# Optimization experiments

Hardware: AMD Instinct MI355X
Metric: run time of the kernel (lower is better)

## Reference

```python
import jax, jax.numpy as jnp
from jax import lax
import numpy as np

N_MACRO, HIDDEN, N_LAYERS, N_REGIMES, N_ASSETS = 16, 256, 2, 3, 32
VIX_THRESHOLD, DEFENSIVE_ALLOC, EPSILON = 30.0, 0.4, 1e-8
N_EQ = 24  # equities = assets[:24], defensive = assets[24:]
N_DEF = N_ASSETS - N_EQ
LN_EPS = 1e-5


def setup_inputs() -> dict:
    key = jax.random.key(0)
    ks = jax.random.split(key, 16)
    B, S = 128, 1024
    inp = {
        'macro_features': jax.random.normal(ks[0], (B, S, N_MACRO), jnp.float32),
        'vix_values': jax.random.uniform(ks[1], (B,), jnp.float32) * 60.0,  # some above threshold
    }
    k = 1.0 / np.sqrt(HIDDEN)
    def u(kk, shape):
        return jax.random.uniform(kk, shape, jnp.float32, -k, k)
    # layer 0
    inp['lstm_Wih0'] = u(ks[2], (4 * HIDDEN, N_MACRO))
    inp['lstm_Whh0'] = u(ks[3], (4 * HIDDEN, HIDDEN))
    inp['lstm_bih0'] = u(ks[4], (4 * HIDDEN,))
    inp['lstm_bhh0'] = u(ks[5], (4 * HIDDEN,))
    # layer 1
    inp['lstm_Wih1'] = u(ks[6], (4 * HIDDEN, HIDDEN))
    inp['lstm_Whh1'] = u(ks[7], (4 * HIDDEN, HIDDEN))
    inp['lstm_bih1'] = u(ks[8], (4 * HIDDEN,))
    inp['lstm_bhh1'] = u(ks[9], (4 * HIDDEN,))
    inp['ln_gamma'] = jnp.ones((HIDDEN,), jnp.float32)
    inp['ln_beta'] = jnp.zeros((HIDDEN,), jnp.float32)
    inp['logits_W'] = u(ks[10], (N_REGIMES, HIDDEN))
    inp['logits_b'] = u(ks[11], (N_REGIMES,))
    inp['risk_budgets'] = jax.random.normal(ks[12], (N_REGIMES, N_ASSETS), jnp.float32) * 0.01
    return inp


def _lstm_layer(x, Wih, Whh, bih, bhh):
    # x: [B,S,I] -> h sequence [B,S,H]
    B = x.shape[0]
    H = Whh.shape[1]
    pre = jnp.einsum('bsi,gi->bsg', x, Wih) + bih + bhh  # [B,S,4H]
    def step(carry, p):
        h, c = carry
        g = p + h @ Whh.T
        i, f, gg, o = jnp.split(g, 4, axis=-1)
        c = jax.nn.sigmoid(f) * c + jax.nn.sigmoid(i) * jnp.tanh(gg)
        h = jax.nn.sigmoid(o) * jnp.tanh(c)
        return (h, c), h
    init = (jnp.zeros((B, H), x.dtype), jnp.zeros((B, H), x.dtype))
    _, hs = lax.scan(step, init, jnp.swapaxes(pre, 0, 1))
    return jnp.swapaxes(hs, 0, 1)


def _vix_override(beta, vix_mask):
    # vectorized version of the per-sample override loop
    eq, df = beta[:, :N_EQ], beta[:, N_EQ:]
    cur_def = df.sum(-1)
    shortfall = DEFENSIVE_ALLOC - cur_def
    eq_total = eq.sum(-1)
    ratio = jnp.minimum(shortfall / jnp.maximum(eq_total, EPSILON), 0.8)
    apply = vix_mask & (shortfall > 0) & (eq_total > EPSILON)
    new_eq = eq * (1.0 - ratio)[:, None]
    new_df = df + (shortfall / N_DEF)[:, None]
    b2 = jnp.concatenate([new_eq, new_df], axis=-1)
    b = jnp.where(apply[:, None], b2, beta)
    b_norm = b / (b.sum(-1, keepdims=True) + EPSILON)
    return jnp.where(vix_mask[:, None], b_norm, beta)


def reference(macro_features, vix_values,
              lstm_Wih0, lstm_Whh0, lstm_bih0, lstm_bhh0,
              lstm_Wih1, lstm_Whh1, lstm_bih1, lstm_bhh1,
              ln_gamma, ln_beta, logits_W, logits_b, risk_budgets):
    h1 = _lstm_layer(macro_features, lstm_Wih0, lstm_Whh0, lstm_bih0, lstm_bhh0)
    h2 = _lstm_layer(h1, lstm_Wih1, lstm_Whh1, lstm_bih1, lstm_bhh1)
    h_last = h2[:, -1, :]  # [B,H]
    mu = h_last.mean(-1, keepdims=True)
    var = ((h_last - mu) ** 2).mean(-1, keepdims=True)
    h_norm = (h_last - mu) / jnp.sqrt(var + LN_EPS) * ln_gamma + ln_beta
    regime_probs = jax.nn.softmax(h_norm @ logits_W.T + logits_b, axis=-1)  # [B,K]
    budgets = jax.nn.softmax(risk_budgets, axis=-1)  # [K,P]
    beta = jnp.einsum('bk,kp->bp', regime_probs, budgets)
    vix_mask = vix_values >= VIX_THRESHOLD
    beta = _vix_override(beta, vix_mask)
    return beta, regime_probs
```

## Files before the change

### kernel.cpp

```cpp
#include <hip/hip_runtime.h>

#define B_  128
#define S_  1024
#define H_  256
#define NM_ 16

typedef short bf16x8 __attribute__((ext_vector_type(8)));
typedef float f32x4  __attribute__((ext_vector_type(4)));

__device__ __forceinline__ short f2bf(float f) {
    unsigned u = __builtin_bit_cast(unsigned, f);
    unsigned r = (u + 0x7FFFu + ((u >> 16) & 1u)) >> 16;
    return (short)r;
}
__device__ __forceinline__ bf16x8 zero8() {
    bf16x8 v;
    #pragma unroll
    for (int j = 0; j < 8; ++j) v[j] = 0;
    return v;
}
__device__ __forceinline__ float sigf(float x)  { return 1.0f / (1.0f + __expf(-x)); }
__device__ __forceinline__ float tanh_(float x) { return 1.0f - 2.0f / (1.0f + __expf(2.0f * x)); }

__device__ __forceinline__ int cload_int(const int* p) {
    int r;
    asm volatile("global_load_dword %0, %1, off sc0 sc1\n\ts_waitcnt vmcnt(0)"
                 : "=v"(r) : "v"(p) : "memory");
    return r;
}
__device__ __forceinline__ void cstore_int(int* p, int v) {
    asm volatile("global_store_dword %0, %1, off sc0 sc1" :: "v"(p), "v"(v) : "memory");
}
__device__ __forceinline__ void cstore_short(short* p, int v) {
    asm volatile("global_store_short %0, %1, off sc0 sc1" :: "v"(p), "v"(v) : "memory");
}
__device__ __forceinline__ void vm_drain() {
    asm volatile("s_waitcnt vmcnt(0)" ::: "memory");
}
__device__ __forceinline__ void cload8x16(const short* p, bf16x8* d) {
    int4 a0, a1, a2, a3, a4, a5, a6, a7;
    asm volatile(
        "global_load_dwordx4 %0, %8, off sc0 sc1\n\t"
        "global_load_dwordx4 %1, %8, off offset:64 sc0 sc1\n\t"
        "global_load_dwordx4 %2, %8, off offset:128 sc0 sc1\n\t"
        "global_load_dwordx4 %3, %8, off offset:192 sc0 sc1\n\t"
        "global_load_dwordx4 %4, %8, off offset:256 sc0 sc1\n\t"
        "global_load_dwordx4 %5, %8, off offset:320 sc0 sc1\n\t"
        "global_load_dwordx4 %6, %8, off offset:384 sc0 sc1\n\t"
        "global_load_dwordx4 %7, %8, off offset:448 sc0 sc1\n\t"
        "s_waitcnt vmcnt(0)"
        : "=&v"(a0), "=&v"(a1), "=&v"(a2), "=&v"(a3),
          "=&v"(a4), "=&v"(a5), "=&v"(a6), "=&v"(a7)
        : "v"(p) : "memory");
    d[0] = __builtin_bit_cast(bf16x8, a0); d[1] = __builtin_bit_cast(bf16x8, a1);
    d[2] = __builtin_bit_cast(bf16x8, a2); d[3] = __builtin_bit_cast(bf16x8, a3);
    d[4] = __builtin_bit_cast(bf16x8, a4); d[5] = __builtin_bit_cast(bf16x8, a5);
    d[6] = __builtin_bit_cast(bf16x8, a6); d[7] = __builtin_bit_cast(bf16x8, a7);
}

__global__ __launch_bounds__(256, 1) void lstm_kernel(
    const float* __restrict__ x,
    const float* __restrict__ Wih0, const float* __restrict__ Whh0,
    const float* __restrict__ bih0, const float* __restrict__ bhh0,
    const float* __restrict__ Wih1, const float* __restrict__ Whh1,
    const float* __restrict__ bih1, const float* __restrict__ bhh1,
    short* __restrict__ h1, short* __restrict__ h2ring,
    float* __restrict__ hlast,
    int* __restrict__ flags0, int* __restrict__ flags1)
{
    const int g    = blockIdx.x & 7;
    const int role = blockIdx.x >> 3;
    const int lane = threadIdx.x & 63;
    const int wv   = threadIdx.x >> 6;
    const int n    = lane & 15;
    const int quad = lane >> 4;

    if (role < 4) {
        const int q = role;
        const int hu_base = q * 64 + wv * 16;
        bf16x8 wf[4][9];
        float  bias[4];
        #pragma unroll
        for (int G = 0; G < 4; ++G) {
            int col = G * 256 + hu_base + n;
            bias[G] = bih0[col] + bhh0[col];
            #pragma unroll
            for (int kt = 0; kt < 8; ++kt) {
                const float* p = Whh0 + (long)col * H_ + kt * 32 + quad * 8;
                bf16x8 v;
                #pragma unroll
                for (int j = 0; j < 8; ++j) v[j] = f2bf(p[j]);
                wf[G][kt] = v;
            }
            bf16x8 v = zero8();
            if (quad < 2) {
                const float* p = Wih0 + (long)col * NM_ + quad * 8;
                #pragma unroll
                for (int j = 0; j < 8; ++j) v[j] = f2bf(p[j]);
            }
            wf[G][8] = v;
        }
        const int  bRow = g * 16 + n;
        const long hA   = (long)bRow * S_ * H_ + quad * 8;
        f32x4 c = {0.f, 0.f, 0.f, 0.f};
        int* fl = flags0 + g * 4;
        for (int t = 0; t < S_; ++t) {
            bf16x8 xfrag = zero8();
            if (quad < 2) {
                const float* p = x + ((long)bRow * S_ + t) * NM_ + quad * 8;
                #pragma unroll
                for (int j = 0; j < 8; ++j) xfrag[j] = f2bf(p[j]);
            }
            if (threadIdx.x < 4) {
                while (cload_int(fl + threadIdx.x) < t) __builtin_amdgcn_s_sleep(1);
            }
            __syncthreads();

            bf16x8 af[9];
            if (t > 0) {
                cload8x16(h1 + hA + (long)(t - 1) * H_, af);
            } else {
                #pragma unroll
                for (int kt = 0; kt < 8; ++kt) af[kt] = zero8();
            }
            af[8] = xfrag;

            f32x4 acc[4];
            #pragma unroll
            for (int G = 0; G < 4; ++G) {
                acc[G][0] = bias[G]; acc[G][1] = bias[G];
                acc[G][2] = bias[G]; acc[G][3] = bias[G];
            }
            #pragma unroll
            for (int kt = 0; kt < 9; ++kt)
                #pragma unroll
                for (int G = 0; G < 4; ++G)
                    acc[G] = __builtin_amdgcn_mfma_f32_16x16x32_bf16(af[kt], wf[G][kt], acc[G], 0, 0, 0);
            #pragma unroll
            for (int r = 0; r < 4; ++r) {
                float iv = sigf(acc[0][r]);
                float fv = sigf(acc[1][r]);
                float gv = tanh_(acc[2][r]);
                float ov = sigf(acc[3][r]);
                c[r] = fv * c[r] + iv * gv;
                float hv = ov * tanh_(c[r]);
                int b = g * 16 + quad * 4 + r;
                cstore_short(h1 + ((long)b * S_ + t) * H_ + hu_base + n, (int)(unsigned short)f2bf(hv));
            }
            vm_drain();
            __syncthreads();
            if (threadIdx.x == 0) cstore_int(fl + q, t + 1);
        }
    } else {
        const int q = role - 4;
        const int hu_base = q * 64 + wv * 16;
        bf16x8 wf[4][16];
        float  bias[4];
        #pragma unroll
        for (int G = 0; G < 4; ++G) {
            int col = G * 256 + hu_base + n;
            bias[G] = bih1[col] + bhh1[col];
            #pragma unroll
            for (int kt = 0; kt < 8; ++kt) {
                const float* p = Whh1 + (long)col * H_ + kt * 32 + quad * 8;
                bf16x8 v;
                #pragma unroll
                for (int j = 0; j < 8; ++j) v[j] = f2bf(p[j]);
                wf[G][kt] = v;
            }
            #pragma unroll
            for (int kt = 0; kt < 8; ++kt) {
                const float* p = Wih1 + (long)col * H_ + kt * 32 + quad * 8;
                bf16x8 v;
                #pragma unroll
                for (int j = 0; j < 8; ++j) v[j] = f2bf(p[j]);
                wf[G][8 + kt] = v;
            }
        }
        const int  bRow = g * 16 + n;
        const long h1A  = (long)bRow * S_ * H_ + quad * 8;
        f32x4 c = {0.f, 0.f, 0.f, 0.f};
        int* fl0 = flags0 + g * 4;
        int* fl1 = flags1 + g * 4;
        for (int t = 0; t < S_; ++t) {
            if (threadIdx.x < 8) {
                const int* fp = (threadIdx.x < 4) ? (fl0 + threadIdx.x) : (fl1 + threadIdx.x - 4);
                const int  tgt = (threadIdx.x < 4) ? (t + 1) : t;
                while (cload_int(fp) < tgt) __builtin_amdgcn_s_sleep(1);
            }
            __syncthreads();

            bf16x8 af[16];
            if (t > 0) {
                cload8x16(h2ring + ((long)bRow * 2 + ((t - 1) & 1)) * H_ + quad * 8, af);
            } else {
                #pragma unroll
                for (int kt = 0; kt < 8; ++kt) af[kt] = zero8();
            }
            cload8x16(h1 + h1A + (long)t * H_, af + 8);

            f32x4 acc[4];
            #pragma unroll
            for (int G = 0; G < 4; ++G) {
                acc[G][0] = bias[G]; acc[G][1] = bias[G];
                acc[G][2] = bias[G]; acc[G][3] = bias[G];
            }
            #pragma unroll
            for (int kt = 0; kt < 16; ++kt)
                #pragma unroll
                for (int G = 0; G < 4; ++G)
                    acc[G] = __builtin_amdgcn_mfma_f32_16x16x32_bf16(af[kt], wf[G][kt], acc[G], 0, 0, 0);
            #pragma unroll
            for (int r = 0; r < 4; ++r) {
                float iv = sigf(acc[0][r]);
                float fv = sigf(acc[1][r]);
                float gv = tanh_(acc[2][r]);
                float ov = sigf(acc[3][r]);
                c[r] = fv * c[r] + iv * gv;
                float hv = ov * tanh_(c[r]);
                int b = g * 16 + quad * 4 + r;
                cstore_short(h2ring + ((long)b * 2 + (t & 1)) * H_ + hu_base + n,
                             (int)(unsigned short)f2bf(hv));
                if (t == S_ - 1) hlast[b * H_ + hu_base + n] = hv;
            }
            vm_drain();
            __syncthreads();
            if (threadIdx.x == 0) cstore_int(fl1 + q, t + 1);
        }
    }
}

__device__ __forceinline__ float blockSum(float v, float* sbuf) {
    #pragma unroll
    for (int off = 32; off > 0; off >>= 1) v += __shfl_down(v, off, 64);
    __syncthreads();
    if ((threadIdx.x & 63) == 0) sbuf[threadIdx.x >> 6] = v;
    __syncthreads();
    return sbuf[0] + sbuf[1] + sbuf[2] + sbuf[3];
}

__global__ __launch_bounds__(256) void tail_kernel(
    const float* __restrict__ hlast, const float* __restrict__ gamma,
    const float* __restrict__ lnbeta, const float* __restrict__ Wl,
    const float* __restrict__ bl, const float* __restrict__ rb,
    const float* __restrict__ vix, float* __restrict__ out)
{
    __shared__ float sbuf[4];
    __shared__ float pr[3], mxs[3], dens[3];
    __shared__ float bvec[32];
    const int b   = blockIdx.x;
    const int tid = threadIdx.x;

    float v  = hlast[b * H_ + tid];
    float mu = blockSum(v, sbuf) * (1.0f / 256.0f);
    float d  = v - mu;
    float var = blockSum(d * d, sbuf) * (1.0f / 256.0f);
    float hn  = d * rsqrtf(var + 1e-5f) * gamma[tid] + lnbeta[tid];

    float l[3];
    #pragma unroll
    for (int k = 0; k < 3; ++k)
        l[k] = blockSum(hn * Wl[k * H_ + tid], sbuf) + bl[k];

    if (tid == 0) {
        float m  = fmaxf(l[0], fmaxf(l[1], l[2]));
        float e0 = __expf(l[0] - m), e1 = __expf(l[1] - m), e2 = __expf(l[2] - m);
        float dn = e0 + e1 + e2;
        pr[0] = e0 / dn; pr[1] = e1 / dn; pr[2] = e2 / dn;
    }
    if (tid < 3) {
        float m = -1e30f;
        for (int p = 0; p < 32; ++p) m = fmaxf(m, rb[tid * 32 + p]);
        float dn = 0.f;
        for (int p = 0; p < 32; ++p) dn += __expf(rb[tid * 32 + p] - m);
        mxs[tid] = m; dens[tid] = dn;
    }
    __syncthreads();
    if (tid < 32) {
        float bp = 0.f;
        #pragma unroll
        for (int k = 0; k < 3; ++k)
            bp += pr[k] * __expf(rb[k * 32 + tid] - mxs[k]) / dens[k];
        bvec[tid] = bp;
    }
    __syncthreads();
    if (tid == 0) {
        bool  mask = vix[b] >= 30.0f;
        float eq_total = 0.f, cur_def = 0.f;
        for (int p = 0; p < 24; ++p) eq_total += bvec[p];
        for (int p = 24; p < 32; ++p) cur_def += bvec[p];
        float shortfall = 0.4f - cur_def;
        float ratio = fminf(shortfall / fmaxf(eq_total, 1e-8f), 0.8f);
        bool  apply = mask && (shortfall > 0.0f) && (eq_total > 1e-8f);
        float bb[32]; float ssum = 0.f;
        for (int p = 0; p < 32; ++p) {
            float b2 = (p < 24) ? bvec[p] * (1.0f - ratio) : bvec[p] + shortfall * (1.0f / 8.0f);
            float bv = apply ? b2 : bvec[p];
            bb[p] = bv; ssum += bv;
        }
        float inv = 1.0f / (ssum + 1e-8f);
        for (int p = 0; p < 32; ++p)
            out[b * 32 + p] = mask ? bb[p] * inv : bvec[p];
        #pragma unroll
        for (int k = 0; k < 3; ++k)
            out[B_ * 32 + b * 3 + k] = pr[k];
    }
}

extern "C" void kernel_launch(void* const* d_in, const int* in_sizes, int n_in,
                              void* d_out, int out_size, void* d_ws, size_t ws_size,
                              hipStream_t stream)
{
    const float* x    = (const float*)d_in[0];
    const float* vix  = (const float*)d_in[1];
    const float* Wih0 = (const float*)d_in[2];
    const float* Whh0 = (const float*)d_in[3];
    const float* bih0 = (const float*)d_in[4];
    const float* bhh0 = (const float*)d_in[5];
    const float* Wih1 = (const float*)d_in[6];
    const float* Whh1 = (const float*)d_in[7];
    const float* bih1 = (const float*)d_in[8];
    const float* bhh1 = (const float*)d_in[9];
    const float* lng  = (const float*)d_in[10];
    const float* lnb  = (const float*)d_in[11];
    const float* Wl   = (const float*)d_in[12];
    const float* bl   = (const float*)d_in[13];
    const float* rb   = (const float*)d_in[14];
    float* out = (float*)d_out;

    char*  ws     = (char*)d_ws;
    short* h1     = (short*)ws;
    int*   flags0 = (int*)(ws + 67108864);
    int*   flags1 = (int*)(ws + 67108864 + 128);
    short* h2ring = (short*)(ws + 67109120);
    float* hlast  = (float*)(ws + 67240192);

    hipMemsetAsync(ws + 67108864, 0, 256, stream);
    lstm_kernel<<<64, 256, 0, stream>>>(x, Wih0, Whh0, bih0, bhh0,
                                        Wih1, Whh1, bih1, bhh1,
                                        h1, h2ring, hlast, flags0, flags1);
    tail_kernel<<<128, 256, 0, stream>>>(hlast, lng, lnb, Wl, bl, rb, vix, out);
}
```

Before: 4.413 ms.

## Replace full h1 sequence buffer with 4-slot ring and pad sync flags

Layer-0 hidden states now go into a 4-deep ring buffer instead of the full 64MB per-timestep array. Layer 0 gains backpressure by waiting on layer-1 flags so it never runs more than three steps ahead. Sync flags are also spaced 128 bytes apart so each lives on its own cache line. The goal is to keep h1 traffic resident in cache and cut flag contention, at the cost of extra polling that couples the two layers more tightly.

```diff
diff --git a/kernel.cpp b/kernel.cpp
--- a/kernel.cpp
+++ b/kernel.cpp
@@ -21,6 +21,9 @@
 }
 __device__ __forceinline__ float sigf(float x)  { return 1.0f / (1.0f + __expf(-x)); }
 __device__ __forceinline__ float tanh_(float x) { return 1.0f - 2.0f / (1.0f + __expf(2.0f * x)); }
+__device__ __forceinline__ void vm_drain() {
+    asm volatile("s_waitcnt vmcnt(0)" ::: "memory");
+}
 
 __device__ __forceinline__ int cload_int(const int* p) {
     int r;
@@ -33,9 +36,6 @@
 }
 __device__ __forceinline__ void cstore_short(short* p, int v) {
     asm volatile("global_store_short %0, %1, off sc0 sc1" :: "v"(p), "v"(v) : "memory");
-}
-__device__ __forceinline__ void vm_drain() {
-    asm volatile("s_waitcnt vmcnt(0)" ::: "memory");
 }
 __device__ __forceinline__ void cload8x16(const short* p, bf16x8* d) {
     int4 a0, a1, a2, a3, a4, a5, a6, a7;
@@ -64,7 +64,7 @@
     const float* __restrict__ bih0, const float* __restrict__ bhh0,
     const float* __restrict__ Wih1, const float* __restrict__ Whh1,
     const float* __restrict__ bih1, const float* __restrict__ bhh1,
-    short* __restrict__ h1, short* __restrict__ h2ring,
+    short* __restrict__ h1ring, short* __restrict__ h2ring,
     float* __restrict__ hlast,
     int* __restrict__ flags0, int* __restrict__ flags1)
 {
@@ -75,6 +75,9 @@
     const int n    = lane & 15;
     const int quad = lane >> 4;
 
+    int* fl0 = flags0 + (g * 4) * 32;
+    int* fl1 = flags1 + (g * 4) * 32;
+
     if (role < 4) {
         const int q = role;
         const int hu_base = q * 64 + wv * 16;
@@ -100,10 +103,8 @@
             }
             wf[G][8] = v;
         }
-        const int  bRow = g * 16 + n;
-        const long hA   = (long)bRow * S_ * H_ + quad * 8;
+        const int bRow = g * 16 + n;
         f32x4 c = {0.f, 0.f, 0.f, 0.f};
-        int* fl = flags0 + g * 4;
         for (int t = 0; t < S_; ++t) {
             bf16x8 xfrag = zero8();
             if (quad < 2) {
@@ -111,14 +112,17 @@
                 #pragma unroll
                 for (int j = 0; j < 8; ++j) xfrag[j] = f2bf(p[j]);
             }
-            if (threadIdx.x < 4) {
-                while (cload_int(fl + threadIdx.x) < t) __builtin_amdgcn_s_sleep(1);
+            if (threadIdx.x < 8) {
+                const int* fp  = (threadIdx.x < 4) ? (fl0 + threadIdx.x * 32)
+                                                   : (fl1 + (threadIdx.x - 4) * 32);
+                const int  tgt = (threadIdx.x < 4) ? t : (t - 3);
+                while (cload_int(fp) < tgt) __builtin_amdgcn_s_sleep(1);
             }
             __syncthreads();
 
             bf16x8 af[9];
             if (t > 0) {
-                cload8x16(h1 + hA + (long)(t - 1) * H_, af);
+                cload8x16(h1ring + (((long)((t - 1) & 3) * B_ + bRow) * H_) + quad * 8, af);
             } else {
                 #pragma unroll
                 for (int kt = 0; kt < 8; ++kt) af[kt] = zero8();
@@ -145,11 +149,12 @@
                 c[r] = fv * c[r] + iv * gv;
                 float hv = ov * tanh_(c[r]);
                 int b = g * 16 + quad * 4 + r;
-                cstore_short(h1 + ((long)b * S_ + t) * H_ + hu_base + n, (int)(unsigned short)f2bf(hv));
+                cstore_short(h1ring + (((long)(t & 3) * B_ + b) * H_) + hu_base + n,
+                             (int)(unsigned short)f2bf(hv));
             }
             vm_drain();
             __syncthreads();
-            if (threadIdx.x == 0) cstore_int(fl + q, t + 1);
+            if (threadIdx.x == 0) cstore_int(fl0 + q * 32, t + 1);
         }
     } else {
         const int q = role - 4;
@@ -177,14 +182,12 @@
                 wf[G][8 + kt] = v;
             }
         }
-        const int  bRow = g * 16 + n;
-        const long h1A  = (long)bRow * S_ * H_ + quad * 8;
+        const int bRow = g * 16 + n;
         f32x4 c = {0.f, 0.f, 0.f, 0.f};
-        int* fl0 = flags0 + g * 4;
-        int* fl1 = flags1 + g * 4;
         for (int t = 0; t < S_; ++t) {
             if (threadIdx.x < 8) {
-                const int* fp = (threadIdx.x < 4) ? (fl0 + threadIdx.x) : (fl1 + threadIdx.x - 4);
+                const int* fp  = (threadIdx.x < 4) ? (fl0 + threadIdx.x * 32)
+                                                   : (fl1 + (threadIdx.x - 4) * 32);
                 const int  tgt = (threadIdx.x < 4) ? (t + 1) : t;
                 while (cload_int(fp) < tgt) __builtin_amdgcn_s_sleep(1);
             }
@@ -197,7 +200,7 @@
                 #pragma unroll
                 for (int kt = 0; kt < 8; ++kt) af[kt] = zero8();
             }
-            cload8x16(h1 + h1A + (long)t * H_, af + 8);
+            cload8x16(h1ring + (((long)(t & 3) * B_ + bRow) * H_) + quad * 8, af + 8);
 
             f32x4 acc[4];
             #pragma unroll
@@ -225,7 +228,7 @@
             }
             vm_drain();
             __syncthreads();
-            if (threadIdx.x == 0) cstore_int(fl1 + q, t + 1);
+            if (threadIdx.x == 0) cstore_int(fl1 + q * 32, t + 1);
         }
     }
 }
@@ -329,15 +332,15 @@
     float* out = (float*)d_out;
 
     char*  ws     = (char*)d_ws;
-    short* h1     = (short*)ws;
-    int*   flags0 = (int*)(ws + 67108864);
-    int*   flags1 = (int*)(ws + 67108864 + 128);
-    short* h2ring = (short*)(ws + 67109120);
-    float* hlast  = (float*)(ws + 67240192);
-
-    hipMemsetAsync(ws + 67108864, 0, 256, stream);
+    short* h1ring = (short*)ws;
+    short* h2ring = (short*)(ws + 262144);
+    float* hlast  = (float*)(ws + 393216);
+    int*   flags0 = (int*)(ws + 524288);
+    int*   flags1 = (int*)(ws + 528384);
+
+    hipMemsetAsync(ws + 524288, 0, 8192, stream);
     lstm_kernel<<<64, 256, 0, stream>>>(x, Wih0, Whh0, bih0, bhh0,
                                         Wih1, Whh1, bih1, bhh1,
-                                        h1, h2ring, hlast, flags0, flags1);
+                                        h1ring, h2ring, hlast, flags0, flags1);
     tail_kernel<<<128, 256, 0, stream>>>(hlast, lng, lnb, Wl, bl, rb, vix, out);
 }
```

Result: faster. 4.124 ms (-6.6%).
